# Optimization experiments

Hardware: AMD Instinct MI355X
Metric: run time of the kernel (lower is better)

The kernel has to match this reference:

```python
import jax, jax.numpy as jnp
import numpy as np

N = 50000    # nodes
E = 800000   # edges
F = 128      # node_feature_dim
H = 128      # GCN hidden
H2 = 64      # fc1 hidden
T = 8        # num_tactics
G = 64       # graphs in batch


def setup_inputs() -> dict:
    key = jax.random.key(0)
    ks = jax.random.split(key, 12)
    s = 0.05
    return {
        "x": jax.random.normal(ks[0], (N, F), jnp.float32),
        "edge_index": jax.random.randint(ks[1], (2, E), 0, N, dtype=jnp.int32),
        "batch": jnp.sort(jax.random.randint(ks[2], (N,), 0, G, dtype=jnp.int32)),
        "W": jax.random.normal(ks[3], (F, H), jnp.float32) * s,
        "b": jax.random.normal(ks[4], (H,), jnp.float32) * s,
        "fc1_w": jax.random.normal(ks[5], (H, H2), jnp.float32) * s,
        "fc1_b": jax.random.normal(ks[6], (H2,), jnp.float32) * s,
        "actor_w": jax.random.normal(ks[7], (H2, T), jnp.float32) * s,
        "actor_b": jax.random.normal(ks[8], (T,), jnp.float32) * s,
        "critic_w": jax.random.normal(ks[9], (H2, 1), jnp.float32) * s,
        "critic_b": jax.random.normal(ks[10], (1,), jnp.float32) * s,
    }


def _gcn_conv(x, edge_index, W, b):
    # PyG GCNConv: add self-loops, symmetric D^-1/2 (A+I) D^-1/2 normalization,
    # linear transform first, then scatter-add aggregation, then bias.
    n = x.shape[0]
    loops = jnp.arange(n, dtype=edge_index.dtype)
    src = jnp.concatenate([edge_index[0], loops])  # message sources (x_j)
    dst = jnp.concatenate([edge_index[1], loops])  # aggregation targets
    deg = jax.ops.segment_sum(jnp.ones_like(dst, jnp.float32), dst, num_segments=N)
    dinv = deg ** -0.5  # deg >= 1 due to self-loops
    norm = dinv[src] * dinv[dst]                   # [E+N]
    h = x @ W                                      # [N, H]
    msgs = h[src] * norm[:, None]                  # [E+N, H]
    return jax.ops.segment_sum(msgs, dst, num_segments=N) + b


def reference(x, edge_index, batch, W, b, fc1_w, fc1_b, actor_w, actor_b, critic_w, critic_b):
    h = jax.nn.relu(_gcn_conv(x, edge_index, W, b))            # [N, H]
    # global_mean_pool over batch index
    sums = jax.ops.segment_sum(h, batch, num_segments=G)       # [G, H]
    cnts = jax.ops.segment_sum(jnp.ones((h.shape[0],), h.dtype), batch, num_segments=G)
    group_state = sums / jnp.maximum(cnts, 1.0)[:, None]
    z = jax.nn.relu(group_state @ fc1_w + fc1_b)               # [G, H2]
    tactic_probs = jax.nn.softmax(z @ actor_w + actor_b, axis=-1)  # [G, T]
    group_value = z @ critic_w + critic_b                      # [G, 1]
    return tactic_probs, group_value
```

## Files before the change

kernel.cpp:

```cpp
#include <hip/hip_runtime.h>
#include <hip/hip_bf16.h>

#define NN 50000
#define EE 800000
#define FF 128
#define HH 128
#define HID2 64
#define TT 8
#define GG 64
#define NB 196
#define NSB 256
#define EPB (EE / NSB)
#define NPAD 50048

using frag_ab = __attribute__((ext_vector_type(8))) short;
using frag_cd = __attribute__((ext_vector_type(4))) float;

__device__ inline unsigned short f2bf(float f) {
    union { float f; unsigned u; } v; v.f = f;
    unsigned r = v.u + 0x7fff + ((v.u >> 16) & 1);
    return (unsigned short)(r >> 16);
}

__global__ __launch_bounds__(256) void k_front(const int* __restrict__ dst,
                                               const float* __restrict__ W,
                                               int* __restrict__ table,
                                               unsigned short* __restrict__ wt_bf,
                                               float* __restrict__ gsum) {
    __shared__ int cnt[NB];
    int t = threadIdx.x, blk = blockIdx.x;
    if (blk < 64) {
        int gid = blk * 256 + t;
        int c = gid >> 7, k = gid & 127;
        wt_bf[gid] = f2bf(W[k * 128 + c]);
    }
    if (blk >= 64 && blk < 96) {
        int gid = (blk - 64) * 256 + t;
        gsum[gid] = 0.f;
    }
    for (int i = t; i < NB; i += 256) cnt[i] = 0;
    __syncthreads();
    int e0 = blk * EPB;
    for (int e = e0 + t; e < e0 + EPB; e += 256)
        atomicAdd(&cnt[dst[e] >> 8], 1);
    __syncthreads();
    for (int i = t; i < NB; i += 256) table[blk * NB + i] = cnt[i];
}

__global__ __launch_bounds__(256) void kb2a(int* __restrict__ table,
                                            int* __restrict__ ctot) {
    __shared__ int s[256];
    int t = threadIdx.x, b = blockIdx.x;
    int v = table[t * NB + b];
    s[t] = v;
    __syncthreads();
    for (int off = 1; off < 256; off <<= 1) {
        int a = s[t];
        int w = (t >= off) ? s[t - off] : 0;
        __syncthreads();
        s[t] = a + w;
        __syncthreads();
    }
    table[t * NB + b] = s[t] - v;
    if (t == 255) ctot[b] = s[255];
}

__global__ __launch_bounds__(256) void kb2b(const int* __restrict__ ctot,
                                            int* __restrict__ bbase) {
    __shared__ int s[256];
    int b = threadIdx.x;
    int v = (b < NB) ? ctot[b] : 0;
    s[b] = v;
    __syncthreads();
    for (int off = 1; off < 256; off <<= 1) {
        int a = s[b];
        int w = (b >= off) ? s[b - off] : 0;
        __syncthreads();
        s[b] = a + w;
        __syncthreads();
    }
    if (b < NB) bbase[b] = s[b] - v;
    if (b == 0) bbase[NB] = EE;
}

__global__ __launch_bounds__(256) void kb3(const int* __restrict__ src,
                                           const int* __restrict__ dst,
                                           const int* __restrict__ table,
                                           const int* __restrict__ bbase,
                                           unsigned* __restrict__ etmp) {
    __shared__ int ofs[NB];
    __shared__ int cur[NB];
    int t = threadIdx.x, blk = blockIdx.x;
    for (int i = t; i < NB; i += 256) {
        ofs[i] = table[blk * NB + i] + bbase[i];
        cur[i] = 0;
    }
    __syncthreads();
    int e0 = blk * EPB;
    for (int e = e0 + t; e < e0 + EPB; e += 256) {
        int d = dst[e];
        int b = d >> 8;
        int r = atomicAdd(&cur[b], 1);
        etmp[ofs[b] + r] = ((unsigned)d << 16) | (unsigned)src[e];
    }
}

__global__ __launch_bounds__(256) void k_csr(const unsigned* __restrict__ etmp,
                                             const int* __restrict__ bbase,
                                             int* __restrict__ row_ptr,
                                             float* __restrict__ dinv,
                                             int* __restrict__ srcs) {
    __shared__ int s[256];
    __shared__ int cur[256];
    int t = threadIdx.x, b = blockIdx.x;
    s[t] = 0;
    __syncthreads();
    int e0 = bbase[b], e1 = bbase[b + 1];
    for (int e = e0 + t; e < e1; e += 256)
        atomicAdd(&s[(etmp[e] >> 16) & 255], 1);
    __syncthreads();
    int v = s[t];
    for (int off = 1; off < 256; off <<= 1) {
        int a = s[t];
        int w = (t >= off) ? s[t - off] : 0;
        __syncthreads();
        s[t] = a + w;
        __syncthreads();
    }
    int excl = s[t] - v + e0;
    int node = b * 256 + t;
    if (node < NN) {
        row_ptr[node] = excl;
        dinv[node] = rsqrtf((float)(v + 1));
    }
    if (b == NB - 1 && t == 0) row_ptr[NN] = EE;
    cur[t] = excl;
    __syncthreads();
    for (int e = e0 + t; e < e1; e += 256) {
        unsigned u = etmp[e];
        int slot = atomicAdd(&cur[(u >> 16) & 255], 1);
        srcs[slot] = (int)(u & 0xffffu);
    }
}

__global__ __launch_bounds__(256) void k_gemm(const float* __restrict__ x,
                                              const unsigned short* __restrict__ wt_bf,
                                              const float* __restrict__ dinv,
                                              unsigned short* __restrict__ hs) {
    int tid = threadIdx.x;
    int w = tid >> 6, lane = tid & 63;
    int m = lane & 15, quad = lane >> 4;
    int r0 = blockIdx.x * 64 + w * 16;
    int row = r0 + m;
    frag_cd acc[8];
#pragma unroll
    for (int nt = 0; nt < 8; nt++) acc[nt] = frag_cd{0.f, 0.f, 0.f, 0.f};

#pragma unroll
    for (int k0 = 0; k0 < 128; k0 += 32) {
        unsigned short av[8];
        if (row < NN) {
            const float4* p = (const float4*)(x + (size_t)row * 128 + k0 + quad * 8);
            float4 a0 = p[0], a1 = p[1];
            av[0] = f2bf(a0.x); av[1] = f2bf(a0.y); av[2] = f2bf(a0.z); av[3] = f2bf(a0.w);
            av[4] = f2bf(a1.x); av[5] = f2bf(a1.y); av[6] = f2bf(a1.z); av[7] = f2bf(a1.w);
        } else {
#pragma unroll
            for (int j = 0; j < 8; j++) av[j] = 0;
        }
        frag_ab a = *(const frag_ab*)av;
#pragma unroll
        for (int nt = 0; nt < 8; nt++) {
            frag_ab bfr = *(const frag_ab*)(wt_bf + (size_t)(nt * 16 + m) * 128 + k0 + quad * 8);
            acc[nt] = __builtin_amdgcn_mfma_f32_16x16x32_bf16(a, bfr, acc[nt], 0, 0, 0);
        }
    }
#pragma unroll
    for (int reg = 0; reg < 4; reg++) {
        int gr = r0 + quad * 4 + reg;
        if (gr < NN) {
            float di = dinv[gr];
#pragma unroll
            for (int nt = 0; nt < 8; nt++)
                hs[(size_t)gr * 128 + nt * 16 + m] = f2bf(acc[nt][reg] * di);
        }
    }
}

#define ACC8(u) \
    a0 += __uint_as_float((u).x << 16); a1 += __uint_as_float((u).x & 0xffff0000u); \
    a2 += __uint_as_float((u).y << 16); a3 += __uint_as_float((u).y & 0xffff0000u); \
    a4 += __uint_as_float((u).z << 16); a5 += __uint_as_float((u).z & 0xffff0000u); \
    a6 += __uint_as_float((u).w << 16); a7 += __uint_as_float((u).w & 0xffff0000u);

__global__ __launch_bounds__(256) void k_aggr(const uint4* __restrict__ hs4,
                                              const int* __restrict__ row_ptr,
                                              const int* __restrict__ srcs,
                                              const float* __restrict__ dinv,
                                              const float* __restrict__ bias,
                                              const int* __restrict__ batch,
                                              float* __restrict__ gsum) {
    __shared__ float gacc[8 * 128];
    int tid = threadIdx.x;
    int qid = tid >> 4, sub = tid & 15;
    int i_base = blockIdx.x * 32;
    int g_first = batch[i_base];
    int last = i_base + 31; if (last >= NN) last = NN - 1;
    int gspan = batch[last] - g_first + 1;
    bool lds_pool = (gspan <= 8);
    int slots = lds_pool ? gspan : 0;
    for (int idx = tid; idx < slots * 128; idx += 256) gacc[idx] = 0.f;
    __syncthreads();

    const float4* b4 = (const float4*)(bias + sub * 8);
    float4 bb0 = b4[0], bb1 = b4[1];

    float racc[8];
#pragma unroll
    for (int j = 0; j < 8; j++) racc[j] = 0.f;
    int cur_lg = -1;

    for (int n = 0; n < 2; n++) {
        int i = i_base + qid * 2 + n;
        if (i >= NN) break;
        int lg = batch[i] - g_first;
        if (lg != cur_lg) {
            if (cur_lg >= 0) {
                float* gp = lds_pool ? &gacc[cur_lg * 128 + sub * 8]
                                     : &gsum[(g_first + cur_lg) * 128 + sub * 8];
#pragma unroll
                for (int j = 0; j < 8; j++) atomicAdd(&gp[j], racc[j]);
#pragma unroll
                for (int j = 0; j < 8; j++) racc[j] = 0.f;
            }
            cur_lg = lg;
        }
        float di = dinv[i];
        uint4 su = hs4[(size_t)i * 16 + sub];
        float a0 = __uint_as_float(su.x << 16);
        float a1 = __uint_as_float(su.x & 0xffff0000u);
        float a2 = __uint_as_float(su.y << 16);
        float a3 = __uint_as_float(su.y & 0xffff0000u);
        float a4 = __uint_as_float(su.z << 16);
        float a5 = __uint_as_float(su.z & 0xffff0000u);
        float a6 = __uint_as_float(su.w << 16);
        float a7 = __uint_as_float(su.w & 0xffff0000u);
        int e = row_ptr[i], e1 = row_ptr[i + 1];
        for (; e + 7 < e1; e += 8) {
            int s0 = srcs[e],     s1 = srcs[e + 1], s2 = srcs[e + 2], s3 = srcs[e + 3];
            int s4 = srcs[e + 4], s5 = srcs[e + 5], s6 = srcs[e + 6], s7 = srcs[e + 7];
            uint4 u0 = hs4[(size_t)s0 * 16 + sub];
            uint4 u1 = hs4[(size_t)s1 * 16 + sub];
            uint4 u2 = hs4[(size_t)s2 * 16 + sub];
            uint4 u3 = hs4[(size_t)s3 * 16 + sub];
            uint4 u4 = hs4[(size_t)s4 * 16 + sub];
            uint4 u5 = hs4[(size_t)s5 * 16 + sub];
            uint4 u6 = hs4[(size_t)s6 * 16 + sub];
            uint4 u7 = hs4[(size_t)s7 * 16 + sub];
            ACC8(u0) ACC8(u1) ACC8(u2) ACC8(u3)
            ACC8(u4) ACC8(u5) ACC8(u6) ACC8(u7)
        }
        for (; e + 3 < e1; e += 4) {
            int s0 = srcs[e], s1 = srcs[e + 1], s2 = srcs[e + 2], s3 = srcs[e + 3];
            uint4 u0 = hs4[(size_t)s0 * 16 + sub];
            uint4 u1 = hs4[(size_t)s1 * 16 + sub];
            uint4 u2 = hs4[(size_t)s2 * 16 + sub];
            uint4 u3 = hs4[(size_t)s3 * 16 + sub];
            ACC8(u0) ACC8(u1) ACC8(u2) ACC8(u3)
        }
        for (; e < e1; ++e) {
            uint4 u0 = hs4[(size_t)srcs[e] * 16 + sub];
            ACC8(u0)
        }
        racc[0] += fmaxf(fmaf(a0, di, bb0.x), 0.f);
        racc[1] += fmaxf(fmaf(a1, di, bb0.y), 0.f);
        racc[2] += fmaxf(fmaf(a2, di, bb0.z), 0.f);
        racc[3] += fmaxf(fmaf(a3, di, bb0.w), 0.f);
        racc[4] += fmaxf(fmaf(a4, di, bb1.x), 0.f);
        racc[5] += fmaxf(fmaf(a5, di, bb1.y), 0.f);
        racc[6] += fmaxf(fmaf(a6, di, bb1.z), 0.f);
        racc[7] += fmaxf(fmaf(a7, di, bb1.w), 0.f);
    }
    if (cur_lg >= 0) {
        float* gp = lds_pool ? &gacc[cur_lg * 128 + sub * 8]
                             : &gsum[(g_first + cur_lg) * 128 + sub * 8];
#pragma unroll
        for (int j = 0; j < 8; j++) atomicAdd(&gp[j], racc[j]);
    }
    __syncthreads();
    for (int idx = tid; idx < slots * 128; idx += 256) {
        float v = gacc[idx];
        if (v != 0.f)
            atomicAdd(&gsum[(g_first + (idx >> 7)) * 128 + (idx & 127)], v);
    }
}

__device__ inline int lbound(const int* __restrict__ a, int n, int key) {
    int lo = 0, hi = n;
    while (lo < hi) {
        int mid = (lo + hi) >> 1;
        if (a[mid] < key) lo = mid + 1;
        else hi = mid;
    }
    return lo;
}

__global__ __launch_bounds__(64) void k_head(const float* __restrict__ gsum,
                                             const int* __restrict__ batch,
                                             const float* __restrict__ fc1_w,
                                             const float* __restrict__ fc1_b,
                                             const float* __restrict__ actor_w,
                                             const float* __restrict__ actor_b,
                                             const float* __restrict__ critic_w,
                                             const float* __restrict__ critic_b,
                                             float* __restrict__ out) {
    __shared__ float gs[128];
    __shared__ float zs[64];
    __shared__ float ls[8], es[8];
    int g = blockIdx.x, t = threadIdx.x;
    int lo = lbound(batch, NN, g), hi = lbound(batch, NN, g + 1);
    float invc = 1.f / fmaxf((float)(hi - lo), 1.f);
    gs[t] = gsum[g * 128 + t] * invc;
    gs[t + 64] = gsum[g * 128 + 64 + t] * invc;
    __syncthreads();
    float z = fc1_b[t];
    for (int k = 0; k < 128; k++) z = fmaf(gs[k], fc1_w[k * 64 + t], z);
    zs[t] = fmaxf(z, 0.f);
    __syncthreads();
    if (t < 8) {
        float l = actor_b[t];
        for (int k = 0; k < 64; k++) l = fmaf(zs[k], actor_w[k * 8 + t], l);
        ls[t] = l;
    }
    __syncthreads();
    if (t < 8) {
        float m = ls[0];
#pragma unroll
        for (int j = 1; j < 8; j++) m = fmaxf(m, ls[j]);
        es[t] = expf(ls[t] - m);
    }
    __syncthreads();
    if (t < 8) {
        float ssum = 0.f;
#pragma unroll
        for (int j = 0; j < 8; j++) ssum += es[j];
        out[g * 8 + t] = es[t] / ssum;
    }
    if (t == 32) {
        float v = critic_b[0];
        for (int k = 0; k < 64; k++) v = fmaf(zs[k], critic_w[k], v);
        out[GG * TT + g] = v;
    }
}

extern "C" void kernel_launch(void* const* d_in, const int* in_sizes, int n_in,
                              void* d_out, int out_size, void* d_ws, size_t ws_size,
                              hipStream_t stream) {
    const float* x        = (const float*)d_in[0];
    const int*   ei       = (const int*)d_in[1];
    const int*   batch    = (const int*)d_in[2];
    const float* W        = (const float*)d_in[3];
    const float* b        = (const float*)d_in[4];
    const float* fc1_w    = (const float*)d_in[5];
    const float* fc1_b    = (const float*)d_in[6];
    const float* actor_w  = (const float*)d_in[7];
    const float* actor_b  = (const float*)d_in[8];
    const float* critic_w = (const float*)d_in[9];
    const float* critic_b = (const float*)d_in[10];
    float* out = (float*)d_out;

    char* ws = (char*)d_ws;
    size_t off = 0;
    unsigned short* hs    = (unsigned short*)(ws + off); off += (size_t)NN * 128 * 2 + 64;
    unsigned short* wt_bf = (unsigned short*)(ws + off); off += (size_t)128 * 128 * 2;
    float* dinv      = (float*)(ws + off);    off += (size_t)NN * 4;
    int*   row_ptr   = (int*)(ws + off);      off += (size_t)(NN + 1) * 4 + 12;
    int*   srcs      = (int*)(ws + off);      off += (size_t)EE * 4;
    unsigned* etmp   = (unsigned*)(ws + off); off += (size_t)EE * 4;
    int*   table     = (int*)(ws + off);      off += (size_t)NSB * NB * 4;
    int*   bbase     = (int*)(ws + off);      off += (size_t)(NB + 1) * 4 + 12;
    int*   ctot      = (int*)(ws + off);      off += (size_t)NB * 4 + 16;
    float* gsum      = (float*)(ws + off);    off += (size_t)GG * HH * 4;

    const int* src = ei;
    const int* dst = ei + EE;

    k_front<<<NSB, 256, 0, stream>>>(dst, W, table, wt_bf, gsum);
    kb2a<<<NB, 256, 0, stream>>>(table, ctot);
    kb2b<<<1, 256, 0, stream>>>(ctot, bbase);
    kb3<<<NSB, 256, 0, stream>>>(src, dst, table, bbase, etmp);
    k_csr<<<NB, 256, 0, stream>>>(etmp, bbase, row_ptr, dinv, srcs);
    k_gemm<<<NPAD / 64, 256, 0, stream>>>(x, wt_bf, dinv, hs);
    k_aggr<<<(NN + 31) / 32, 256, 0, stream>>>((const uint4*)hs, row_ptr, srcs,
                                               dinv, b, batch, gsum);
    k_head<<<GG, 64, 0, stream>>>(gsum, batch, fc1_w, fc1_b, actor_w, actor_b,
                                  critic_w, critic_b, out);
}
```

Before: 196.0 us.

## Fuse CSR build kernels into one persistent kernel with grid barriers; one node per aggr group

Merges the five CSR-construction launches (histogram, two scans, scatter, per-bucket sort) into a single kernel of 256 co-resident blocks separated by atomic-counter grid barriers. This removes four kernel launch gaps at the cost of spin-waiting, and it relies on all blocks being resident at once. The aggregation kernel also changes from two nodes per 16-lane group to one node per group, doubling the grid size. It drops the 8-wide unroll and accumulates into the pool directly with atomics, exposing more parallelism in exchange for more atomic traffic.

Result: slower. 284.1 us (+44.9%).

```diff
diff --git a/kernel.cpp b/kernel.cpp
--- a/kernel.cpp
+++ b/kernel.cpp
@@ -22,124 +22,138 @@
     return (unsigned short)(r >> 16);
 }
 
-__global__ __launch_bounds__(256) void k_front(const int* __restrict__ dst,
+__device__ inline void gbar(int* __restrict__ bar, int idx) {
+    __syncthreads();
+    if (threadIdx.x == 0) {
+        __threadfence();
+        atomicAdd(&bar[idx], 1);
+        while (__hip_atomic_load(&bar[idx], __ATOMIC_RELAXED,
+                                 __HIP_MEMORY_SCOPE_AGENT) < NSB) {
+            __builtin_amdgcn_s_sleep(1);
+        }
+        __threadfence();
+    }
+    __syncthreads();
+}
+
+__global__ __launch_bounds__(256) void k_build(const int* __restrict__ src,
+                                               const int* __restrict__ dst,
                                                const float* __restrict__ W,
                                                int* __restrict__ table,
+                                               int* __restrict__ ctot,
+                                               int* __restrict__ bbase,
+                                               unsigned* __restrict__ etmp,
+                                               int* __restrict__ row_ptr,
+                                               float* __restrict__ dinv,
+                                               int* __restrict__ srcs,
                                                unsigned short* __restrict__ wt_bf,
-                                               float* __restrict__ gsum) {
-    __shared__ int cnt[NB];
+                                               float* __restrict__ gsum,
+                                               int* __restrict__ bar) {
+    __shared__ int shm[512];
     int t = threadIdx.x, blk = blockIdx.x;
+
     if (blk < 64) {
         int gid = blk * 256 + t;
         int c = gid >> 7, k = gid & 127;
         wt_bf[gid] = f2bf(W[k * 128 + c]);
-    }
-    if (blk >= 64 && blk < 96) {
+    } else if (blk < 96) {
         int gid = (blk - 64) * 256 + t;
         gsum[gid] = 0.f;
     }
-    for (int i = t; i < NB; i += 256) cnt[i] = 0;
-    __syncthreads();
-    int e0 = blk * EPB;
-    for (int e = e0 + t; e < e0 + EPB; e += 256)
-        atomicAdd(&cnt[dst[e] >> 8], 1);
-    __syncthreads();
-    for (int i = t; i < NB; i += 256) table[blk * NB + i] = cnt[i];
-}
-
-__global__ __launch_bounds__(256) void kb2a(int* __restrict__ table,
-                                            int* __restrict__ ctot) {
-    __shared__ int s[256];
-    int t = threadIdx.x, b = blockIdx.x;
-    int v = table[t * NB + b];
-    s[t] = v;
-    __syncthreads();
-    for (int off = 1; off < 256; off <<= 1) {
-        int a = s[t];
-        int w = (t >= off) ? s[t - off] : 0;
-        __syncthreads();
-        s[t] = a + w;
-        __syncthreads();
-    }
-    table[t * NB + b] = s[t] - v;
-    if (t == 255) ctot[b] = s[255];
-}
-
-__global__ __launch_bounds__(256) void kb2b(const int* __restrict__ ctot,
-                                            int* __restrict__ bbase) {
-    __shared__ int s[256];
-    int b = threadIdx.x;
-    int v = (b < NB) ? ctot[b] : 0;
-    s[b] = v;
-    __syncthreads();
-    for (int off = 1; off < 256; off <<= 1) {
-        int a = s[b];
-        int w = (b >= off) ? s[b - off] : 0;
-        __syncthreads();
-        s[b] = a + w;
-        __syncthreads();
-    }
-    if (b < NB) bbase[b] = s[b] - v;
-    if (b == 0) bbase[NB] = EE;
-}
-
-__global__ __launch_bounds__(256) void kb3(const int* __restrict__ src,
-                                           const int* __restrict__ dst,
-                                           const int* __restrict__ table,
-                                           const int* __restrict__ bbase,
-                                           unsigned* __restrict__ etmp) {
-    __shared__ int ofs[NB];
-    __shared__ int cur[NB];
-    int t = threadIdx.x, blk = blockIdx.x;
-    for (int i = t; i < NB; i += 256) {
-        ofs[i] = table[blk * NB + i] + bbase[i];
-        cur[i] = 0;
-    }
-    __syncthreads();
-    int e0 = blk * EPB;
-    for (int e = e0 + t; e < e0 + EPB; e += 256) {
-        int d = dst[e];
-        int b = d >> 8;
-        int r = atomicAdd(&cur[b], 1);
-        etmp[ofs[b] + r] = ((unsigned)d << 16) | (unsigned)src[e];
-    }
-}
-
-__global__ __launch_bounds__(256) void k_csr(const unsigned* __restrict__ etmp,
-                                             const int* __restrict__ bbase,
-                                             int* __restrict__ row_ptr,
-                                             float* __restrict__ dinv,
-                                             int* __restrict__ srcs) {
-    __shared__ int s[256];
-    __shared__ int cur[256];
-    int t = threadIdx.x, b = blockIdx.x;
-    s[t] = 0;
-    __syncthreads();
-    int e0 = bbase[b], e1 = bbase[b + 1];
-    for (int e = e0 + t; e < e1; e += 256)
-        atomicAdd(&s[(etmp[e] >> 16) & 255], 1);
-    __syncthreads();
-    int v = s[t];
-    for (int off = 1; off < 256; off <<= 1) {
-        int a = s[t];
-        int w = (t >= off) ? s[t - off] : 0;
-        __syncthreads();
-        s[t] = a + w;
-        __syncthreads();
-    }
-    int excl = s[t] - v + e0;
-    int node = b * 256 + t;
-    if (node < NN) {
-        row_ptr[node] = excl;
-        dinv[node] = rsqrtf((float)(v + 1));
-    }
-    if (b == NB - 1 && t == 0) row_ptr[NN] = EE;
-    cur[t] = excl;
-    __syncthreads();
-    for (int e = e0 + t; e < e1; e += 256) {
-        unsigned u = etmp[e];
-        int slot = atomicAdd(&cur[(u >> 16) & 255], 1);
-        srcs[slot] = (int)(u & 0xffffu);
+    for (int i = t; i < NB; i += 256) shm[i] = 0;
+    __syncthreads();
+    {
+        int e0 = blk * EPB;
+        for (int e = e0 + t; e < e0 + EPB; e += 256)
+            atomicAdd(&shm[dst[e] >> 8], 1);
+    }
+    __syncthreads();
+    for (int i = t; i < NB; i += 256) table[blk * NB + i] = shm[i];
+    gbar(bar, 0);
+
+    if (blk < NB) {
+        int b = blk;
+        int v = table[t * NB + b];
+        shm[t] = v;
+        __syncthreads();
+        for (int off = 1; off < 256; off <<= 1) {
+            int a = shm[t];
+            int w = (t >= off) ? shm[t - off] : 0;
+            __syncthreads();
+            shm[t] = a + w;
+            __syncthreads();
+        }
+        table[t * NB + b] = shm[t] - v;
+        if (t == 255) ctot[b] = shm[255];
+    }
+    gbar(bar, 1);
+
+    if (blk == 0) {
+        int v = (t < NB) ? ctot[t] : 0;
+        shm[t] = v;
+        __syncthreads();
+        for (int off = 1; off < 256; off <<= 1) {
+            int a = shm[t];
+            int w = (t >= off) ? shm[t - off] : 0;
+            __syncthreads();
+            shm[t] = a + w;
+            __syncthreads();
+        }
+        if (t < NB) bbase[t] = shm[t] - v;
+        if (t == 0) bbase[NB] = EE;
+    }
+    gbar(bar, 2);
+
+    {
+        int* ofs = shm;
+        int* cur = shm + 256;
+        for (int i = t; i < NB; i += 256) {
+            ofs[i] = table[blk * NB + i] + bbase[i];
+            cur[i] = 0;
+        }
+        __syncthreads();
+        int e0 = blk * EPB;
+        for (int e = e0 + t; e < e0 + EPB; e += 256) {
+            int d = dst[e];
+            int b = d >> 8;
+            int r = atomicAdd(&cur[b], 1);
+            etmp[ofs[b] + r] = ((unsigned)d << 16) | (unsigned)src[e];
+        }
+    }
+    gbar(bar, 3);
+
+    if (blk < NB) {
+        int b = blk;
+        int* s = shm;
+        int* cur = shm + 256;
+        s[t] = 0;
+        __syncthreads();
+        int e0 = bbase[b], e1 = bbase[b + 1];
+        for (int e = e0 + t; e < e1; e += 256)
+            atomicAdd(&s[(etmp[e] >> 16) & 255], 1);
+        __syncthreads();
+        int v = s[t];
+        for (int off = 1; off < 256; off <<= 1) {
+            int a = s[t];
+            int w = (t >= off) ? s[t - off] : 0;
+            __syncthreads();
+            s[t] = a + w;
+            __syncthreads();
+        }
+        int excl = s[t] - v + e0;
+        int node = b * 256 + t;
+        if (node < NN) {
+            row_ptr[node] = excl;
+            dinv[node] = rsqrtf((float)(v + 1));
+        }
+        if (b == NB - 1 && t == 0) row_ptr[NN] = EE;
+        cur[t] = excl;
+        __syncthreads();
+        for (int e = e0 + t; e < e1; e += 256) {
+            unsigned u = etmp[e];
+            int slot = atomicAdd(&cur[(u >> 16) & 255], 1);
+            srcs[slot] = (int)(u & 0xffffu);
+        }
     }
 }
 
@@ -203,9 +217,10 @@
     __shared__ float gacc[8 * 128];
     int tid = threadIdx.x;
     int qid = tid >> 4, sub = tid & 15;
-    int i_base = blockIdx.x * 32;
+    int i_base = blockIdx.x * 16;
+    int i = i_base + qid;
     int g_first = batch[i_base];
-    int last = i_base + 31; if (last >= NN) last = NN - 1;
+    int last = i_base + 15; if (last >= NN) last = NN - 1;
     int gspan = batch[last] - g_first + 1;
     bool lds_pool = (gspan <= 8);
     int slots = lds_pool ? gspan : 0;
@@ -215,78 +230,44 @@
     const float4* b4 = (const float4*)(bias + sub * 8);
     float4 bb0 = b4[0], bb1 = b4[1];
 
-    float racc[8];
-#pragma unroll
-    for (int j = 0; j < 8; j++) racc[j] = 0.f;
-    int cur_lg = -1;
-
-    for (int n = 0; n < 2; n++) {
-        int i = i_base + qid * 2 + n;
-        if (i >= NN) break;
-        int lg = batch[i] - g_first;
-        if (lg != cur_lg) {
-            if (cur_lg >= 0) {
-                float* gp = lds_pool ? &gacc[cur_lg * 128 + sub * 8]
-                                     : &gsum[(g_first + cur_lg) * 128 + sub * 8];
-#pragma unroll
-                for (int j = 0; j < 8; j++) atomicAdd(&gp[j], racc[j]);
-#pragma unroll
-                for (int j = 0; j < 8; j++) racc[j] = 0.f;
-            }
-            cur_lg = lg;
-        }
-        float di = dinv[i];
-        uint4 su = hs4[(size_t)i * 16 + sub];
-        float a0 = __uint_as_float(su.x << 16);
-        float a1 = __uint_as_float(su.x & 0xffff0000u);
-        float a2 = __uint_as_float(su.y << 16);
-        float a3 = __uint_as_float(su.y & 0xffff0000u);
-        float a4 = __uint_as_float(su.z << 16);
-        float a5 = __uint_as_float(su.z & 0xffff0000u);
-        float a6 = __uint_as_float(su.w << 16);
-        float a7 = __uint_as_float(su.w & 0xffff0000u);
-        int e = row_ptr[i], e1 = row_ptr[i + 1];
-        for (; e + 7 < e1; e += 8) {
-            int s0 = srcs[e],     s1 = srcs[e + 1], s2 = srcs[e + 2], s3 = srcs[e + 3];
-            int s4 = srcs[e + 4], s5 = srcs[e + 5], s6 = srcs[e + 6], s7 = srcs[e + 7];
-            uint4 u0 = hs4[(size_t)s0 * 16 + sub];
-            uint4 u1 = hs4[(size_t)s1 * 16 + sub];
-            uint4 u2 = hs4[(size_t)s2 * 16 + sub];
-            uint4 u3 = hs4[(size_t)s3 * 16 + sub];
-            uint4 u4 = hs4[(size_t)s4 * 16 + sub];
-            uint4 u5 = hs4[(size_t)s5 * 16 + sub];
-            uint4 u6 = hs4[(size_t)s6 * 16 + sub];
-            uint4 u7 = hs4[(size_t)s7 * 16 + sub];
-            ACC8(u0) ACC8(u1) ACC8(u2) ACC8(u3)
-            ACC8(u4) ACC8(u5) ACC8(u6) ACC8(u7)
-        }
-        for (; e + 3 < e1; e += 4) {
-            int s0 = srcs[e], s1 = srcs[e + 1], s2 = srcs[e + 2], s3 = srcs[e + 3];
-            uint4 u0 = hs4[(size_t)s0 * 16 + sub];
-            uint4 u1 = hs4[(size_t)s1 * 16 + sub];
-            uint4 u2 = hs4[(size_t)s2 * 16 + sub];
-            uint4 u3 = hs4[(size_t)s3 * 16 + sub];
-            ACC8(u0) ACC8(u1) ACC8(u2) ACC8(u3)
-        }
-        for (; e < e1; ++e) {
-            uint4 u0 = hs4[(size_t)srcs[e] * 16 + sub];
-            ACC8(u0)
-        }
-        racc[0] += fmaxf(fmaf(a0, di, bb0.x), 0.f);
-        racc[1] += fmaxf(fmaf(a1, di, bb0.y), 0.f);
-        racc[2] += fmaxf(fmaf(a2, di, bb0.z), 0.f);
-        racc[3] += fmaxf(fmaf(a3, di, bb0.w), 0.f);
-        racc[4] += fmaxf(fmaf(a4, di, bb1.x), 0.f);
-        racc[5] += fmaxf(fmaf(a5, di, bb1.y), 0.f);
-        racc[6] += fmaxf(fmaf(a6, di, bb1.z), 0.f);
-        racc[7] += fmaxf(fmaf(a7, di, bb1.w), 0.f);
-    }
-    if (cur_lg >= 0) {
-        float* gp = lds_pool ? &gacc[cur_lg * 128 + sub * 8]
-                             : &gsum[(g_first + cur_lg) * 128 + sub * 8];
-#pragma unroll
-        for (int j = 0; j < 8; j++) atomicAdd(&gp[j], racc[j]);
-    }
+    float di = dinv[i];
+    uint4 su = hs4[(size_t)i * 16 + sub];
+    float a0 = __uint_as_float(su.x << 16);
+    float a1 = __uint_as_float(su.x & 0xffff0000u);
+    float a2 = __uint_as_float(su.y << 16);
+    float a3 = __uint_as_float(su.y & 0xffff0000u);
+    float a4 = __uint_as_float(su.z << 16);
+    float a5 = __uint_as_float(su.z & 0xffff0000u);
+    float a6 = __uint_as_float(su.w << 16);
+    float a7 = __uint_as_float(su.w & 0xffff0000u);
+    int e = row_ptr[i], e1 = row_ptr[i + 1];
+    for (; e + 3 < e1; e += 4) {
+        int s0 = srcs[e], s1 = srcs[e + 1], s2 = srcs[e + 2], s3 = srcs[e + 3];
+        uint4 u0 = hs4[(size_t)s0 * 16 + sub];
+        uint4 u1 = hs4[(size_t)s1 * 16 + sub];
+        uint4 u2 = hs4[(size_t)s2 * 16 + sub];
+        uint4 u3 = hs4[(size_t)s3 * 16 + sub];
+        ACC8(u0) ACC8(u1) ACC8(u2) ACC8(u3)
+    }
+    for (; e < e1; ++e) {
+        uint4 u0 = hs4[(size_t)srcs[e] * 16 + sub];
+        ACC8(u0)
+    }
+    float r0 = fmaxf(fmaf(a0, di, bb0.x), 0.f);
+    float r1 = fmaxf(fmaf(a1, di, bb0.y), 0.f);
+    float r2 = fmaxf(fmaf(a2, di, bb0.z), 0.f);
+    float r3 = fmaxf(fmaf(a3, di, bb0.w), 0.f);
+    float r4 = fmaxf(fmaf(a4, di, bb1.x), 0.f);
+    float r5 = fmaxf(fmaf(a5, di, bb1.y), 0.f);
+    float r6 = fmaxf(fmaf(a6, di, bb1.z), 0.f);
+    float r7 = fmaxf(fmaf(a7, di, bb1.w), 0.f);
+    int lg = batch[i] - g_first;
+    float* gp = lds_pool ? &gacc[lg * 128 + sub * 8]
+                         : &gsum[(g_first + lg) * 128 + sub * 8];
+    atomicAdd(&gp[0], r0); atomicAdd(&gp[1], r1);
+    atomicAdd(&gp[2], r2); atomicAdd(&gp[3], r3);
+    atomicAdd(&gp[4], r4); atomicAdd(&gp[5], r5);
+    atomicAdd(&gp[6], r6); atomicAdd(&gp[7], r7);
     __syncthreads();
     for (int idx = tid; idx < slots * 128; idx += 256) {
         float v = gacc[idx];
@@ -381,18 +362,17 @@
     int*   bbase     = (int*)(ws + off);      off += (size_t)(NB + 1) * 4 + 12;
     int*   ctot      = (int*)(ws + off);      off += (size_t)NB * 4 + 16;
     float* gsum      = (float*)(ws + off);    off += (size_t)GG * HH * 4;
+    int*   bar       = (int*)(ws + off);      off += 64;
 
     const int* src = ei;
     const int* dst = ei + EE;
 
-    k_front<<<NSB, 256, 0, stream>>>(dst, W, table, wt_bf, gsum);
-    kb2a<<<NB, 256, 0, stream>>>(table, ctot);
-    kb2b<<<1, 256, 0, stream>>>(ctot, bbase);
-    kb3<<<NSB, 256, 0, stream>>>(src, dst, table, bbase, etmp);
-    k_csr<<<NB, 256, 0, stream>>>(etmp, bbase, row_ptr, dinv, srcs);
+    hipMemsetAsync(bar, 0, 64, stream);
+    k_build<<<NSB, 256, 0, stream>>>(src, dst, W, table, ctot, bbase, etmp,
+                                     row_ptr, dinv, srcs, wt_bf, gsum, bar);
     k_gemm<<<NPAD / 64, 256, 0, stream>>>(x, wt_bf, dinv, hs);
-    k_aggr<<<(NN + 31) / 32, 256, 0, stream>>>((const uint4*)hs, row_ptr, srcs,
-                                               dinv, b, batch, gsum);
+    k_aggr<<<NN / 16, 256, 0, stream>>>((const uint4*)hs, row_ptr, srcs,
+                                        dinv, b, batch, gsum);
     k_head<<<GG, 64, 0, stream>>>(gsum, batch, fc1_w, fc1_b, actor_w, actor_b,
                                   critic_w, critic_b, out);
 }
```

## Split hidden features into four 32-column slabs and aggregate each slab separately

Applied to the files above, without the earlier changes.

The GEMM output is stored as four feature slabs of 32 columns each (column-blocked layout), and the aggregation kernel runs four times, once per slab, with four threads per node instead of sixteen. The intent is to make each slab's gather working set (about 3.2 MB) fit in cache so random neighbour reads hit L2/MALL more often. The cost is that the CSR indices and row pointers are read four times, there are extra kernel launches, and the 8-way edge unroll is dropped.

Result: slower. 233.0 us (+18.9%).

```diff
diff --git a/kernel.cpp b/kernel.cpp
--- a/kernel.cpp
+++ b/kernel.cpp
@@ -12,6 +12,7 @@
 #define NSB 256
 #define EPB (EE / NSB)
 #define NPAD 50048
+#define SLABU ((size_t)NN * 32)
 
 using frag_ab = __attribute__((ext_vector_type(8))) short;
 using frag_cd = __attribute__((ext_vector_type(4))) float;
@@ -146,7 +147,7 @@
 __global__ __launch_bounds__(256) void k_gemm(const float* __restrict__ x,
                                               const unsigned short* __restrict__ wt_bf,
                                               const float* __restrict__ dinv,
-                                              unsigned short* __restrict__ hs) {
+                                              unsigned short* __restrict__ hsq) {
     int tid = threadIdx.x;
     int w = tid >> 6, lane = tid & 63;
     int m = lane & 15, quad = lane >> 4;
@@ -181,8 +182,11 @@
         if (gr < NN) {
             float di = dinv[gr];
 #pragma unroll
-            for (int nt = 0; nt < 8; nt++)
-                hs[(size_t)gr * 128 + nt * 16 + m] = f2bf(acc[nt][reg] * di);
+            for (int nt = 0; nt < 8; nt++) {
+                int c = nt * 16 + m;
+                hsq[(size_t)(c >> 5) * SLABU + (size_t)gr * 32 + (c & 31)] =
+                    f2bf(acc[nt][reg] * di);
+            }
         }
     }
 }
@@ -193,50 +197,31 @@
     a4 += __uint_as_float((u).z << 16); a5 += __uint_as_float((u).z & 0xffff0000u); \
     a6 += __uint_as_float((u).w << 16); a7 += __uint_as_float((u).w & 0xffff0000u);
 
-__global__ __launch_bounds__(256) void k_aggr(const uint4* __restrict__ hs4,
-                                              const int* __restrict__ row_ptr,
-                                              const int* __restrict__ srcs,
-                                              const float* __restrict__ dinv,
-                                              const float* __restrict__ bias,
-                                              const int* __restrict__ batch,
-                                              float* __restrict__ gsum) {
-    __shared__ float gacc[8 * 128];
-    int tid = threadIdx.x;
-    int qid = tid >> 4, sub = tid & 15;
-    int i_base = blockIdx.x * 32;
+__global__ __launch_bounds__(256) void k_aggrq(const uint4* __restrict__ slab4,
+                                               const int* __restrict__ row_ptr,
+                                               const int* __restrict__ srcs,
+                                               const float* __restrict__ dinv,
+                                               const float* __restrict__ bias_q,
+                                               const int* __restrict__ batch,
+                                               float* __restrict__ gsum_q) {
+    __shared__ float gacc[8 * 32];
+    int t = threadIdx.x;
+    int grp = t >> 2, j = t & 3;
+    int i_base = blockIdx.x * 64;
+    int node = i_base + grp;
+    int last = i_base + 63; if (last >= NN) last = NN - 1;
     int g_first = batch[i_base];
-    int last = i_base + 31; if (last >= NN) last = NN - 1;
     int gspan = batch[last] - g_first + 1;
     bool lds_pool = (gspan <= 8);
     int slots = lds_pool ? gspan : 0;
-    for (int idx = tid; idx < slots * 128; idx += 256) gacc[idx] = 0.f;
-    __syncthreads();
-
-    const float4* b4 = (const float4*)(bias + sub * 8);
-    float4 bb0 = b4[0], bb1 = b4[1];
-
-    float racc[8];
-#pragma unroll
-    for (int j = 0; j < 8; j++) racc[j] = 0.f;
-    int cur_lg = -1;
-
-    for (int n = 0; n < 2; n++) {
-        int i = i_base + qid * 2 + n;
-        if (i >= NN) break;
-        int lg = batch[i] - g_first;
-        if (lg != cur_lg) {
-            if (cur_lg >= 0) {
-                float* gp = lds_pool ? &gacc[cur_lg * 128 + sub * 8]
-                                     : &gsum[(g_first + cur_lg) * 128 + sub * 8];
-#pragma unroll
-                for (int j = 0; j < 8; j++) atomicAdd(&gp[j], racc[j]);
-#pragma unroll
-                for (int j = 0; j < 8; j++) racc[j] = 0.f;
-            }
-            cur_lg = lg;
-        }
-        float di = dinv[i];
-        uint4 su = hs4[(size_t)i * 16 + sub];
+    if (t < slots * 32) gacc[t] = 0.f;
+    __syncthreads();
+
+    if (node < NN) {
+        const float4* b4 = (const float4*)(bias_q + j * 8);
+        float4 bb0 = b4[0], bb1 = b4[1];
+        float di = dinv[node];
+        uint4 su = slab4[(size_t)node * 4 + j];
         float a0 = __uint_as_float(su.x << 16);
         float a1 = __uint_as_float(su.x & 0xffff0000u);
         float a2 = __uint_as_float(su.y << 16);
@@ -245,53 +230,40 @@
         float a5 = __uint_as_float(su.z & 0xffff0000u);
         float a6 = __uint_as_float(su.w << 16);
         float a7 = __uint_as_float(su.w & 0xffff0000u);
-        int e = row_ptr[i], e1 = row_ptr[i + 1];
-        for (; e + 7 < e1; e += 8) {
-            int s0 = srcs[e],     s1 = srcs[e + 1], s2 = srcs[e + 2], s3 = srcs[e + 3];
-            int s4 = srcs[e + 4], s5 = srcs[e + 5], s6 = srcs[e + 6], s7 = srcs[e + 7];
-            uint4 u0 = hs4[(size_t)s0 * 16 + sub];
-            uint4 u1 = hs4[(size_t)s1 * 16 + sub];
-            uint4 u2 = hs4[(size_t)s2 * 16 + sub];
-            uint4 u3 = hs4[(size_t)s3 * 16 + sub];
-            uint4 u4 = hs4[(size_t)s4 * 16 + sub];
-            uint4 u5 = hs4[(size_t)s5 * 16 + sub];
-            uint4 u6 = hs4[(size_t)s6 * 16 + sub];
-            uint4 u7 = hs4[(size_t)s7 * 16 + sub];
-            ACC8(u0) ACC8(u1) ACC8(u2) ACC8(u3)
-            ACC8(u4) ACC8(u5) ACC8(u6) ACC8(u7)
-        }
+        int e = row_ptr[node], e1 = row_ptr[node + 1];
         for (; e + 3 < e1; e += 4) {
             int s0 = srcs[e], s1 = srcs[e + 1], s2 = srcs[e + 2], s3 = srcs[e + 3];
-            uint4 u0 = hs4[(size_t)s0 * 16 + sub];
-            uint4 u1 = hs4[(size_t)s1 * 16 + sub];
-            uint4 u2 = hs4[(size_t)s2 * 16 + sub];
-            uint4 u3 = hs4[(size_t)s3 * 16 + sub];
+            uint4 u0 = slab4[(size_t)s0 * 4 + j];
+            uint4 u1 = slab4[(size_t)s1 * 4 + j];
+            uint4 u2 = slab4[(size_t)s2 * 4 + j];
+            uint4 u3 = slab4[(size_t)s3 * 4 + j];
             ACC8(u0) ACC8(u1) ACC8(u2) ACC8(u3)
         }
         for (; e < e1; ++e) {
-            uint4 u0 = hs4[(size_t)srcs[e] * 16 + sub];
+            uint4 u0 = slab4[(size_t)srcs[e] * 4 + j];
             ACC8(u0)
         }
-        racc[0] += fmaxf(fmaf(a0, di, bb0.x), 0.f);
-        racc[1] += fmaxf(fmaf(a1, di, bb0.y), 0.f);
-        racc[2] += fmaxf(fmaf(a2, di, bb0.z), 0.f);
-        racc[3] += fmaxf(fmaf(a3, di, bb0.w), 0.f);
-        racc[4] += fmaxf(fmaf(a4, di, bb1.x), 0.f);
-        racc[5] += fmaxf(fmaf(a5, di, bb1.y), 0.f);
-        racc[6] += fmaxf(fmaf(a6, di, bb1.z), 0.f);
-        racc[7] += fmaxf(fmaf(a7, di, bb1.w), 0.f);
-    }
-    if (cur_lg >= 0) {
-        float* gp = lds_pool ? &gacc[cur_lg * 128 + sub * 8]
-                             : &gsum[(g_first + cur_lg) * 128 + sub * 8];
-#pragma unroll
-        for (int j = 0; j < 8; j++) atomicAdd(&gp[j], racc[j]);
-    }
-    __syncthreads();
-    for (int idx = tid; idx < slots * 128; idx += 256) {
-        float v = gacc[idx];
+        float r0 = fmaxf(fmaf(a0, di, bb0.x), 0.f);
+        float r1 = fmaxf(fmaf(a1, di, bb0.y), 0.f);
+        float r2 = fmaxf(fmaf(a2, di, bb0.z), 0.f);
+        float r3 = fmaxf(fmaf(a3, di, bb0.w), 0.f);
+        float r4 = fmaxf(fmaf(a4, di, bb1.x), 0.f);
+        float r5 = fmaxf(fmaf(a5, di, bb1.y), 0.f);
+        float r6 = fmaxf(fmaf(a6, di, bb1.z), 0.f);
+        float r7 = fmaxf(fmaf(a7, di, bb1.w), 0.f);
+        int lg = batch[node] - g_first;
+        float* gp = lds_pool ? &gacc[lg * 32 + j * 8]
+                             : &gsum_q[(g_first + lg) * 128 + j * 8];
+        atomicAdd(&gp[0], r0); atomicAdd(&gp[1], r1);
+        atomicAdd(&gp[2], r2); atomicAdd(&gp[3], r3);
+        atomicAdd(&gp[4], r4); atomicAdd(&gp[5], r5);
+        atomicAdd(&gp[6], r6); atomicAdd(&gp[7], r7);
+    }
+    __syncthreads();
+    if (t < slots * 32) {
+        float v = gacc[t];
         if (v != 0.f)
-            atomicAdd(&gsum[(g_first + (idx >> 7)) * 128 + (idx & 127)], v);
+            atomicAdd(&gsum_q[(g_first + (t >> 5)) * 128 + (t & 31)], v);
     }
 }
 
@@ -371,7 +343,7 @@
 
     char* ws = (char*)d_ws;
     size_t off = 0;
-    unsigned short* hs    = (unsigned short*)(ws + off); off += (size_t)NN * 128 * 2 + 64;
+    unsigned short* hsq   = (unsigned short*)(ws + off); off += (size_t)NN * 128 * 2 + 64;
     unsigned short* wt_bf = (unsigned short*)(ws + off); off += (size_t)128 * 128 * 2;
     float* dinv      = (float*)(ws + off);    off += (size_t)NN * 4;
     int*   row_ptr   = (int*)(ws + off);      off += (size_t)(NN + 1) * 4 + 12;
@@ -390,9 +362,12 @@
     kb2b<<<1, 256, 0, stream>>>(ctot, bbase);
     kb3<<<NSB, 256, 0, stream>>>(src, dst, table, bbase, etmp);
     k_csr<<<NB, 256, 0, stream>>>(etmp, bbase, row_ptr, dinv, srcs);
-    k_gemm<<<NPAD / 64, 256, 0, stream>>>(x, wt_bf, dinv, hs);
-    k_aggr<<<(NN + 31) / 32, 256, 0, stream>>>((const uint4*)hs, row_ptr, srcs,
-                                               dinv, b, batch, gsum);
+    k_gemm<<<NPAD / 64, 256, 0, stream>>>(x, wt_bf, dinv, hsq);
+    for (int q = 0; q < 4; q++) {
+        k_aggrq<<<NPAD / 64, 256, 0, stream>>>(
+            (const uint4*)(hsq + (size_t)q * SLABU), row_ptr, srcs, dinv,
+            b + q * 32, batch, gsum + q * 32);
+    }
     k_head<<<GG, 64, 0, stream>>>(gsum, batch, fc1_w, fc1_b, actor_w, actor_b,
                                   critic_w, critic_b, out);
 }
```

## Give each aggregation thread-group one node, use 16-bit source indices, per-wave histograms

Applied to the files above, without the earlier changes.

The aggregation kernel now assigns one node per 16-lane group (16 nodes per block, twice as many blocks) instead of two nodes walked in sequence. This raises parallelism and memory-level concurrency for the gather, and the 8-wide unrolled edge loop is dropped. The CSR source index array is stored as 16-bit values, which halves index traffic, and the front histogram uses per-wavefront LDS copies to reduce atomic contention. In exchange, each node now issues its own pooling atomics. The block size also relies on NN being divisible by 16 with no bounds check.

After: 201.8 us. 1.03x slower.

```diff
diff --git a/kernel.cpp b/kernel.cpp
--- a/kernel.cpp
+++ b/kernel.cpp
@@ -27,8 +27,9 @@
                                                int* __restrict__ table,
                                                unsigned short* __restrict__ wt_bf,
                                                float* __restrict__ gsum) {
-    __shared__ int cnt[NB];
+    __shared__ int cnt[4 * NB];
     int t = threadIdx.x, blk = blockIdx.x;
+    int wv = t >> 6;
     if (blk < 64) {
         int gid = blk * 256 + t;
         int c = gid >> 7, k = gid & 127;
@@ -38,13 +39,15 @@
         int gid = (blk - 64) * 256 + t;
         gsum[gid] = 0.f;
     }
-    for (int i = t; i < NB; i += 256) cnt[i] = 0;
+    for (int i = t; i < 4 * NB; i += 256) cnt[i] = 0;
     __syncthreads();
     int e0 = blk * EPB;
+    int* my = cnt + wv * NB;
     for (int e = e0 + t; e < e0 + EPB; e += 256)
-        atomicAdd(&cnt[dst[e] >> 8], 1);
-    __syncthreads();
-    for (int i = t; i < NB; i += 256) table[blk * NB + i] = cnt[i];
+        atomicAdd(&my[dst[e] >> 8], 1);
+    __syncthreads();
+    for (int i = t; i < NB; i += 256)
+        table[blk * NB + i] = cnt[i] + cnt[NB + i] + cnt[2 * NB + i] + cnt[3 * NB + i];
 }
 
 __global__ __launch_bounds__(256) void kb2a(int* __restrict__ table,
@@ -109,7 +112,7 @@
                                              const int* __restrict__ bbase,
                                              int* __restrict__ row_ptr,
                                              float* __restrict__ dinv,
-                                             int* __restrict__ srcs) {
+                                             unsigned short* __restrict__ srcs) {
     __shared__ int s[256];
     __shared__ int cur[256];
     int t = threadIdx.x, b = blockIdx.x;
@@ -139,7 +142,7 @@
     for (int e = e0 + t; e < e1; e += 256) {
         unsigned u = etmp[e];
         int slot = atomicAdd(&cur[(u >> 16) & 255], 1);
-        srcs[slot] = (int)(u & 0xffffu);
+        srcs[slot] = (unsigned short)(u & 0xffffu);
     }
 }
 
@@ -195,7 +198,7 @@
 
 __global__ __launch_bounds__(256) void k_aggr(const uint4* __restrict__ hs4,
                                               const int* __restrict__ row_ptr,
-                                              const int* __restrict__ srcs,
+                                              const unsigned short* __restrict__ srcs,
                                               const float* __restrict__ dinv,
                                               const float* __restrict__ bias,
                                               const int* __restrict__ batch,
@@ -203,10 +206,10 @@
     __shared__ float gacc[8 * 128];
     int tid = threadIdx.x;
     int qid = tid >> 4, sub = tid & 15;
-    int i_base = blockIdx.x * 32;
+    int i_base = blockIdx.x * 16;
+    int i = i_base + qid;
     int g_first = batch[i_base];
-    int last = i_base + 31; if (last >= NN) last = NN - 1;
-    int gspan = batch[last] - g_first + 1;
+    int gspan = batch[i_base + 15] - g_first + 1;
     bool lds_pool = (gspan <= 8);
     int slots = lds_pool ? gspan : 0;
     for (int idx = tid; idx < slots * 128; idx += 256) gacc[idx] = 0.f;
@@ -215,78 +218,44 @@
     const float4* b4 = (const float4*)(bias + sub * 8);
     float4 bb0 = b4[0], bb1 = b4[1];
 
-    float racc[8];
-#pragma unroll
-    for (int j = 0; j < 8; j++) racc[j] = 0.f;
-    int cur_lg = -1;
-
-    for (int n = 0; n < 2; n++) {
-        int i = i_base + qid * 2 + n;
-        if (i >= NN) break;
-        int lg = batch[i] - g_first;
-        if (lg != cur_lg) {
-            if (cur_lg >= 0) {
-                float* gp = lds_pool ? &gacc[cur_lg * 128 + sub * 8]
-                                     : &gsum[(g_first + cur_lg) * 128 + sub * 8];
-#pragma unroll
-                for (int j = 0; j < 8; j++) atomicAdd(&gp[j], racc[j]);
-#pragma unroll
-                for (int j = 0; j < 8; j++) racc[j] = 0.f;
-            }
-            cur_lg = lg;
-        }
-        float di = dinv[i];
-        uint4 su = hs4[(size_t)i * 16 + sub];
-        float a0 = __uint_as_float(su.x << 16);
-        float a1 = __uint_as_float(su.x & 0xffff0000u);
-        float a2 = __uint_as_float(su.y << 16);
-        float a3 = __uint_as_float(su.y & 0xffff0000u);
-        float a4 = __uint_as_float(su.z << 16);
-        float a5 = __uint_as_float(su.z & 0xffff0000u);
-        float a6 = __uint_as_float(su.w << 16);
-        float a7 = __uint_as_float(su.w & 0xffff0000u);
-        int e = row_ptr[i], e1 = row_ptr[i + 1];
-        for (; e + 7 < e1; e += 8) {
-            int s0 = srcs[e],     s1 = srcs[e + 1], s2 = srcs[e + 2], s3 = srcs[e + 3];
-            int s4 = srcs[e + 4], s5 = srcs[e + 5], s6 = srcs[e + 6], s7 = srcs[e + 7];
-            uint4 u0 = hs4[(size_t)s0 * 16 + sub];
-            uint4 u1 = hs4[(size_t)s1 * 16 + sub];
-            uint4 u2 = hs4[(size_t)s2 * 16 + sub];
-            uint4 u3 = hs4[(size_t)s3 * 16 + sub];
-            uint4 u4 = hs4[(size_t)s4 * 16 + sub];
-            uint4 u5 = hs4[(size_t)s5 * 16 + sub];
-            uint4 u6 = hs4[(size_t)s6 * 16 + sub];
-            uint4 u7 = hs4[(size_t)s7 * 16 + sub];
-            ACC8(u0) ACC8(u1) ACC8(u2) ACC8(u3)
-            ACC8(u4) ACC8(u5) ACC8(u6) ACC8(u7)
-        }
-        for (; e + 3 < e1; e += 4) {
-            int s0 = srcs[e], s1 = srcs[e + 1], s2 = srcs[e + 2], s3 = srcs[e + 3];
-            uint4 u0 = hs4[(size_t)s0 * 16 + sub];
-            uint4 u1 = hs4[(size_t)s1 * 16 + sub];
-            uint4 u2 = hs4[(size_t)s2 * 16 + sub];
-            uint4 u3 = hs4[(size_t)s3 * 16 + sub];
-            ACC8(u0) ACC8(u1) ACC8(u2) ACC8(u3)
-        }
-        for (; e < e1; ++e) {
-            uint4 u0 = hs4[(size_t)srcs[e] * 16 + sub];
-            ACC8(u0)
-        }
-        racc[0] += fmaxf(fmaf(a0, di, bb0.x), 0.f);
-        racc[1] += fmaxf(fmaf(a1, di, bb0.y), 0.f);
-        racc[2] += fmaxf(fmaf(a2, di, bb0.z), 0.f);
-        racc[3] += fmaxf(fmaf(a3, di, bb0.w), 0.f);
-        racc[4] += fmaxf(fmaf(a4, di, bb1.x), 0.f);
-        racc[5] += fmaxf(fmaf(a5, di, bb1.y), 0.f);
-        racc[6] += fmaxf(fmaf(a6, di, bb1.z), 0.f);
-        racc[7] += fmaxf(fmaf(a7, di, bb1.w), 0.f);
-    }
-    if (cur_lg >= 0) {
-        float* gp = lds_pool ? &gacc[cur_lg * 128 + sub * 8]
-                             : &gsum[(g_first + cur_lg) * 128 + sub * 8];
-#pragma unroll
-        for (int j = 0; j < 8; j++) atomicAdd(&gp[j], racc[j]);
-    }
+    float di = dinv[i];
+    uint4 su = hs4[(size_t)i * 16 + sub];
+    float a0 = __uint_as_float(su.x << 16);
+    float a1 = __uint_as_float(su.x & 0xffff0000u);
+    float a2 = __uint_as_float(su.y << 16);
+    float a3 = __uint_as_float(su.y & 0xffff0000u);
+    float a4 = __uint_as_float(su.z << 16);
+    float a5 = __uint_as_float(su.z & 0xffff0000u);
+    float a6 = __uint_as_float(su.w << 16);
+    float a7 = __uint_as_float(su.w & 0xffff0000u);
+    int e = row_ptr[i], e1 = row_ptr[i + 1];
+    for (; e + 3 < e1; e += 4) {
+        int s0 = srcs[e], s1 = srcs[e + 1], s2 = srcs[e + 2], s3 = srcs[e + 3];
+        uint4 u0 = hs4[(size_t)s0 * 16 + sub];
+        uint4 u1 = hs4[(size_t)s1 * 16 + sub];
+        uint4 u2 = hs4[(size_t)s2 * 16 + sub];
+        uint4 u3 = hs4[(size_t)s3 * 16 + sub];
+        ACC8(u0) ACC8(u1) ACC8(u2) ACC8(u3)
+    }
+    for (; e < e1; ++e) {
+        uint4 u0 = hs4[(size_t)srcs[e] * 16 + sub];
+        ACC8(u0)
+    }
+    float r0 = fmaxf(fmaf(a0, di, bb0.x), 0.f);
+    float r1 = fmaxf(fmaf(a1, di, bb0.y), 0.f);
+    float r2 = fmaxf(fmaf(a2, di, bb0.z), 0.f);
+    float r3 = fmaxf(fmaf(a3, di, bb0.w), 0.f);
+    float r4 = fmaxf(fmaf(a4, di, bb1.x), 0.f);
+    float r5 = fmaxf(fmaf(a5, di, bb1.y), 0.f);
+    float r6 = fmaxf(fmaf(a6, di, bb1.z), 0.f);
+    float r7 = fmaxf(fmaf(a7, di, bb1.w), 0.f);
+    int lg = batch[i] - g_first;
+    float* gp = lds_pool ? &gacc[lg * 128 + sub * 8]
+                         : &gsum[(g_first + lg) * 128 + sub * 8];
+    atomicAdd(&gp[0], r0); atomicAdd(&gp[1], r1);
+    atomicAdd(&gp[2], r2); atomicAdd(&gp[3], r3);
+    atomicAdd(&gp[4], r4); atomicAdd(&gp[5], r5);
+    atomicAdd(&gp[6], r6); atomicAdd(&gp[7], r7);
     __syncthreads();
     for (int idx = tid; idx < slots * 128; idx += 256) {
         float v = gacc[idx];
@@ -375,7 +344,7 @@
     unsigned short* wt_bf = (unsigned short*)(ws + off); off += (size_t)128 * 128 * 2;
     float* dinv      = (float*)(ws + off);    off += (size_t)NN * 4;
     int*   row_ptr   = (int*)(ws + off);      off += (size_t)(NN + 1) * 4 + 12;
-    int*   srcs      = (int*)(ws + off);      off += (size_t)EE * 4;
+    unsigned short* srcs = (unsigned short*)(ws + off); off += (size_t)EE * 2 + 32;
     unsigned* etmp   = (unsigned*)(ws + off); off += (size_t)EE * 4;
     int*   table     = (int*)(ws + off);      off += (size_t)NSB * NB * 4;
     int*   bbase     = (int*)(ws + off);      off += (size_t)(NB + 1) * 4 + 12;
@@ -391,8 +360,8 @@
     kb3<<<NSB, 256, 0, stream>>>(src, dst, table, bbase, etmp);
     k_csr<<<NB, 256, 0, stream>>>(etmp, bbase, row_ptr, dinv, srcs);
     k_gemm<<<NPAD / 64, 256, 0, stream>>>(x, wt_bf, dinv, hs);
-    k_aggr<<<(NN + 31) / 32, 256, 0, stream>>>((const uint4*)hs, row_ptr, srcs,
-                                               dinv, b, batch, gsum);
+    k_aggr<<<NN / 16, 256, 0, stream>>>((const uint4*)hs, row_ptr, srcs,
+                                        dinv, b, batch, gsum);
     k_head<<<GG, 64, 0, stream>>>(gsum, batch, fc1_w, fc1_b, actor_w, actor_b,
                                   critic_w, critic_b, out);
 }
```
